# Kernel optimization log

Hardware: AMD Instinct MI355X
Metric: run time of the kernel (lower is better)

## Reference

```python
import jax, jax.numpy as jnp
import numpy as np

X_MIN, X_MAX = -2.0, 2.0


def _pchip_slopes_uniform(y, h):
    # y: [..., K], uniform knot spacing h. Fritsch-Carlson / PCHIP slopes.
    delta = (y[..., 1:] - y[..., :-1]) / h            # [..., K-1]
    dp, dn = delta[..., :-1], delta[..., 1:]          # [..., K-2]
    same_sign = dp * dn > 0
    d_mid = jnp.where(same_sign, 2.0 * dp * dn / (dp + dn + 1e-12), 0.0)

    def _fix_endpoint(d_end, delta0, delta1):
        d_end = jnp.where(d_end * delta0 <= 0, 0.0, d_end)
        d_end = jnp.where((delta0 * delta1 < 0) & (jnp.abs(d_end) > 3.0 * jnp.abs(delta0)),
                          3.0 * delta0, d_end)
        return d_end

    d0 = _fix_endpoint((3.0 * delta[..., 0] - delta[..., 1]) / 2.0, delta[..., 0], delta[..., 1])
    dN = _fix_endpoint((3.0 * delta[..., -1] - delta[..., -2]) / 2.0, delta[..., -1], delta[..., -2])
    return jnp.concatenate([d0[..., None], d_mid, dN[..., None]], axis=-1)


def setup_inputs() -> dict:
    key = jax.random.key(0)
    k1, k2 = jax.random.split(key)
    B, O, D, K = 8192, 64, 64, 64
    x = jax.random.normal(k1, (B, D), dtype=jnp.float32)
    coeffs = 0.01 * jax.random.normal(k2, (O, D, K), dtype=jnp.float32)
    bias = jnp.zeros((O,), dtype=jnp.float32)
    return {"x": x, "coeffs": coeffs, "bias": bias}


def reference(x, coeffs, bias):
    # x: [B, D]; coeffs: [O, D, K]; bias: [O] -> out: [B, O]
    O, D, K = coeffs.shape
    h = (X_MAX - X_MIN) / (K - 1)
    slopes = _pchip_slopes_uniform(coeffs, h)          # [O, D, K]

    t = (x - X_MIN) / h                                # [B, D]
    idx = jnp.clip(jnp.floor(t).astype(jnp.int32), 0, K - 2)
    u = (t - idx)[None]                                # [1, B, D]

    darange = jnp.arange(D)[None, :]                   # broadcasts with idx [B, D]
    y0 = coeffs[:, darange, idx]                       # [O, B, D]
    y1 = coeffs[:, darange, idx + 1]
    d0 = slopes[:, darange, idx]
    d1 = slopes[:, darange, idx + 1]

    u2 = u * u
    u3 = u2 * u
    h00 = 2.0 * u3 - 3.0 * u2 + 1.0
    h10 = u3 - 2.0 * u2 + u
    h01 = -2.0 * u3 + 3.0 * u2
    h11 = u3 - u2
    interp = h00 * y0 + h10 * (h * d0) + h01 * y1 + h11 * (h * d1)  # [O, B, D]

    # linear extrapolation outside [X_MIN, X_MAX]
    left = coeffs[:, :, 0][:, None, :] + slopes[:, :, 0][:, None, :] * (x - X_MIN)[None]
    right = coeffs[:, :, -1][:, None, :] + slopes[:, :, -1][:, None, :] * (x - X_MAX)[None]
    interp = jnp.where((x < X_MIN)[None], left, interp)
    interp = jnp.where((x > X_MAX)[None], right, interp)

    out = interp.sum(axis=-1).T + bias[None, :]        # [B, O]
    return out
```

## Files before the change

kernel.cpp:

```cpp
#include <hip/hip_runtime.h>
#include <hip/hip_fp16.h>
#include <stdint.h>


typedef _Float16 half2v __attribute__((ext_vector_type(2)));

#if defined(__has_builtin)
#if __has_builtin(__builtin_amdgcn_fdot2)
#define HAS_FDOT2 1
#endif
#endif

__device__ __forceinline__ uint32_t h16(float f) {
    return (uint32_t)__half_as_ushort(__float2half(f));
}

__device__ __forceinline__ float dot2acc(uint32_t a_bits, uint32_t b_bits, float acc) {
    half2v a = __builtin_bit_cast(half2v, a_bits);
    half2v b = __builtin_bit_cast(half2v, b_bits);
#ifdef HAS_FDOT2
    return __builtin_amdgcn_fdot2(a, b, acc, false);
#else
    return acc + (float)a.x * (float)b.x + (float)a.y * (float)b.y;
#endif
}

__global__ void build_table(const float* __restrict__ coeffs, uint2* __restrict__ T) {
    const float hf = 4.0f / 63.0f;
    const float inv_hf = 63.0f / 4.0f;
    int d  = blockIdx.x >> 2;
    int ob = (blockIdx.x & 3) << 4;
    __shared__ float Y[16][65];
    int t = threadIdx.x;
    {
        int ol = t >> 4;
        int k4 = (t & 15) << 2;
        const float* src = coeffs + (size_t)(ob + ol) * 4096 + d * 64 + k4;
        float4 v = *(const float4*)src;
        Y[ol][k4 + 0] = v.x; Y[ol][k4 + 1] = v.y;
        Y[ol][k4 + 2] = v.z; Y[ol][k4 + 3] = v.w;
    }
    __syncthreads();
    for (int c = t; c < 1024; c += 256) {
        int ol = c & 15;
        int i  = c >> 4;
        const float* Yr = Y[ol];
        auto delt = [&](int k) -> float { return (Yr[k + 1] - Yr[k]) * inv_hf; };
        auto endslope = [&](float a, float b) -> float {
            float de = (3.0f * a - b) * 0.5f;
            de = (de * a <= 0.0f) ? 0.0f : de;
            de = ((a * b < 0.0f) && (fabsf(de) > 3.0f * fabsf(a))) ? 3.0f * a : de;
            return de;
        };
        auto slope = [&](int k) -> float {
            if (k == 0)  return endslope(delt(0), delt(1));
            if (k == 63) return endslope(delt(62), delt(61));
            float dp = delt(k - 1), dn = delt(k);
            return (dp * dn > 0.0f) ? (2.0f * dp * dn) / (dp + dn + 1e-12f) : 0.0f;
        };
        uint2 pk;
        if (i < 63) {
            float y0 = Yr[i], y1 = Yr[i + 1];
            float di = slope(i), dj = slope(i + 1);
            float c0 = y0;
            float c1 = hf * di;
            float c2 = 3.0f * (y1 - y0) - hf * (2.0f * di + dj);
            float c3 = 2.0f * (y0 - y1) + hf * (di + dj);
            pk.x = (h16(c1) << 16) | h16(c0);
            pk.y = (h16(c3) << 16) | h16(c2);
        } else {
            float yN = Yr[63];
            float dN = slope(63);
            pk.x = (h16(hf * dN) << 16) | h16(yN);
            pk.y = 0u;
        }
        T[(size_t)d * 4096 + i * 64 + (ob + ol)] = pk;
    }
}

__global__ void __launch_bounds__(256) kan_main(const float* __restrict__ x,
                                                const float* __restrict__ bias,
                                                const char* __restrict__ Tb,
                                                float* __restrict__ out) {
    __shared__ uint4 WL[256];
    int t    = threadIdx.x;
    int lane = t & 63;
    int wv   = t >> 6;
    int b    = blockIdx.x * 4 + wv;

    {
        float xv = x[b * 64 + lane];
        float tt = (xv + 2.0f) * 15.75f;
        int i = (int)floorf(tt);
        i = i < 0 ? 0 : (i > 62 ? 62 : i);
        float u = tt - (float)i;
        float w1, w2, w3; uint32_t off;
        if (xv < -2.0f)      { w1 = tt;          w2 = 0.f;    w3 = 0.f;    off = 0u; }
        else if (xv > 2.0f)  { w1 = tt - 63.0f;  w2 = 0.f;    w3 = 0.f;    off = 63u << 9; }
        else                 { w1 = u;           w2 = u * u;  w3 = w2 * u; off = (uint32_t)i << 9; }
        half2v wa; wa.x = (_Float16)1.0f; wa.y = (_Float16)w1;
        half2v wb; wb.x = (_Float16)w2;   wb.y = (_Float16)w3;
        uint32_t full_off = ((uint32_t)lane << 15) | off;
        WL[t] = make_uint4(__builtin_bit_cast(uint32_t, wa),
                           __builtin_bit_cast(uint32_t, wb), full_off, 0u);
    }
    __syncthreads();

    float acc0 = bias[lane];
    float acc1 = 0.0f;
    int laneoff = lane << 3;
    const uint4* wl = &WL[wv << 6];
    #pragma unroll 8
    for (int d = 0; d < 64; ++d) {
        uint4 q = wl[d];
        uint32_t off = __builtin_amdgcn_readfirstlane(q.z);
        uint2 c = *(const uint2*)(Tb + off + laneoff);
        acc0 = dot2acc(q.x, c.x, acc0);
        acc1 = dot2acc(q.y, c.y, acc1);
    }
    out[b * 64 + lane] = acc0 + acc1;
}

extern "C" void kernel_launch(void* const* d_in, const int* in_sizes, int n_in,
                              void* d_out, int out_size, void* d_ws, size_t ws_size,
                              hipStream_t stream) {
    const float* x      = (const float*)d_in[0];
    const float* coeffs = (const float*)d_in[1];
    const float* bias   = (const float*)d_in[2];
    float* out = (float*)d_out;

    uint2* T = (uint2*)d_ws;
    build_table<<<dim3(256), dim3(256), 0, stream>>>(coeffs, T);
    kan_main<<<dim3(2048), dim3(256), 0, stream>>>(x, bias, (const char*)d_ws, out);
}
```

Measured before the change: 79.06 us.

## Split each batch row's D reduction across four waves using readlane broadcasts

Each block now handles one batch row instead of four. Its four waves each cover 16 of the 64 input dimensions and combine partial sums through shared memory. Per-dimension weights and offsets are broadcast with readlane instead of being staged in LDS, which removes the LDS weight table and the pre-loop barrier. This raises the grid to 8192 blocks, shortens each wave's serial dependency chain and fully unrolls it, at the cost of a final barrier, an LDS reduction and three idle waves during the store.

```diff
diff --git a/kernel.cpp b/kernel.cpp
--- a/kernel.cpp
+++ b/kernel.cpp
@@ -82,12 +82,13 @@
                                                 const float* __restrict__ bias,
                                                 const char* __restrict__ Tb,
                                                 float* __restrict__ out) {
-    __shared__ uint4 WL[256];
+    __shared__ float R[4][64];
     int t    = threadIdx.x;
     int lane = t & 63;
     int wv   = t >> 6;
-    int b    = blockIdx.x * 4 + wv;
+    int b    = blockIdx.x;
 
+    uint32_t wa_bits, wb_bits, off_full;
     {
         float xv = x[b * 64 + lane];
         float tt = (xv + 2.0f) * 15.75f;
@@ -100,25 +101,32 @@
         else                 { w1 = u;           w2 = u * u;  w3 = w2 * u; off = (uint32_t)i << 9; }
         half2v wa; wa.x = (_Float16)1.0f; wa.y = (_Float16)w1;
         half2v wb; wb.x = (_Float16)w2;   wb.y = (_Float16)w3;
-        uint32_t full_off = ((uint32_t)lane << 15) | off;
-        WL[t] = make_uint4(__builtin_bit_cast(uint32_t, wa),
-                           __builtin_bit_cast(uint32_t, wb), full_off, 0u);
+        wa_bits  = __builtin_bit_cast(uint32_t, wa);
+        wb_bits  = __builtin_bit_cast(uint32_t, wb);
+        off_full = ((uint32_t)lane << 15) | off;
     }
-    __syncthreads();
 
-    float acc0 = bias[lane];
+    float acc0 = 0.0f;
     float acc1 = 0.0f;
     int laneoff = lane << 3;
-    const uint4* wl = &WL[wv << 6];
-    #pragma unroll 8
-    for (int d = 0; d < 64; ++d) {
-        uint4 q = wl[d];
-        uint32_t off = __builtin_amdgcn_readfirstlane(q.z);
+    int lb = __builtin_amdgcn_readfirstlane(wv << 4);
+    #pragma unroll
+    for (int j = 0; j < 16; ++j) {
+        int src = lb + j;
+        uint32_t qa  = (uint32_t)__builtin_amdgcn_readlane((int)wa_bits,  src);
+        uint32_t qb  = (uint32_t)__builtin_amdgcn_readlane((int)wb_bits,  src);
+        uint32_t off = (uint32_t)__builtin_amdgcn_readlane((int)off_full, src);
         uint2 c = *(const uint2*)(Tb + off + laneoff);
-        acc0 = dot2acc(q.x, c.x, acc0);
-        acc1 = dot2acc(q.y, c.y, acc1);
+        acc0 = dot2acc(qa, c.x, acc0);
+        acc1 = dot2acc(qb, c.y, acc1);
     }
-    out[b * 64 + lane] = acc0 + acc1;
+
+    R[wv][lane] = acc0 + acc1;
+    __syncthreads();
+    if (wv == 0) {
+        float r = R[0][lane] + R[1][lane] + R[2][lane] + R[3][lane] + bias[lane];
+        out[b * 64 + lane] = r;
+    }
 }
 
 extern "C" void kernel_launch(void* const* d_in, const int* in_sizes, int n_in,
@@ -131,5 +139,5 @@
 
     uint2* T = (uint2*)d_ws;
     build_table<<<dim3(256), dim3(256), 0, stream>>>(coeffs, T);
-    kan_main<<<dim3(2048), dim3(256), 0, stream>>>(x, bias, (const char*)d_ws, out);
+    kan_main<<<dim3(8192), dim3(256), 0, stream>>>(x, bias, (const char*)d_ws, out);
 }
```

Measured after the change: 80.24 us. About the same (+1.5%).

## Stage coefficient table slices in LDS and split D across blocks with reduction

Applied to the files above, without the earlier changes.

The main kernel now splits the D dimension into 8 groups per block. Each block copies 2-dimension slices of the packed Hermite table into LDS with global_load_lds, then evaluates 256 batch rows against that LDS-resident table instead of gathering from global memory per element. Partial sums per D group go to a workspace and a new reduce kernel adds them together with the bias. The intent is to replace scattered global/L2 gathers with LDS reads and more reuse per block. The cost is an extra kernel launch, extra traffic for the partials, 64KB+ of LDS per block (lower occupancy), and barriers around each table reload.

```diff
diff --git a/kernel.cpp b/kernel.cpp
--- a/kernel.cpp
+++ b/kernel.cpp
@@ -78,47 +78,104 @@
     }
 }
 
-__global__ void __launch_bounds__(256) kan_main(const float* __restrict__ x,
-                                                const float* __restrict__ bias,
+__global__ void __launch_bounds__(512) kan_main(const float* __restrict__ x,
                                                 const char* __restrict__ Tb,
-                                                float* __restrict__ out) {
-    __shared__ uint4 WL[256];
-    int t    = threadIdx.x;
-    int lane = t & 63;
-    int wv   = t >> 6;
-    int b    = blockIdx.x * 4 + wv;
+                                                float* __restrict__ part) {
+    __shared__ char  TL[65536];
+    __shared__ uint4 REC[256][8];
+
+    const int t     = threadIdx.x;
+    const int lane  = t & 63;
+    const int wv    = t >> 6;
+    const int p     = blockIdx.x & 7;
+    const int btile = blockIdx.x >> 3;
+    const int dg    = p << 3;
+    const int bbase = btile << 8;
 
     {
-        float xv = x[b * 64 + lane];
+        const char* src = Tb + ((size_t)dg << 15);
+        #pragma unroll
+        for (int r = 0; r < 8; ++r) {
+            __builtin_amdgcn_global_load_lds(
+                (const uint32_t*)(src + t * 16 + r * 8192),
+                (uint32_t*)(TL + t * 16 + r * 8192), 16, 0, 0);
+        }
+    }
+
+    #pragma unroll
+    for (int k = 0; k < 4; ++k) {
+        int r  = t + (k << 9);
+        int bl = r >> 3;
+        int dl = r & 7;
+        float xv = x[(bbase + bl) * 64 + dg + dl];
         float tt = (xv + 2.0f) * 15.75f;
         int i = (int)floorf(tt);
         i = i < 0 ? 0 : (i > 62 ? 62 : i);
         float u = tt - (float)i;
         float w1, w2, w3; uint32_t off;
-        if (xv < -2.0f)      { w1 = tt;          w2 = 0.f;    w3 = 0.f;    off = 0u; }
-        else if (xv > 2.0f)  { w1 = tt - 63.0f;  w2 = 0.f;    w3 = 0.f;    off = 63u << 9; }
-        else                 { w1 = u;           w2 = u * u;  w3 = w2 * u; off = (uint32_t)i << 9; }
+        if (xv < -2.0f)      { w1 = tt;          w2 = 0.f;    w3 = 0.f;     off = 0u; }
+        else if (xv > 2.0f)  { w1 = tt - 63.0f;  w2 = 0.f;    w3 = 0.f;     off = 63u << 9; }
+        else                 { w1 = u;           w2 = u * u;  w3 = w2 * u;  off = (uint32_t)i << 9; }
         half2v wa; wa.x = (_Float16)1.0f; wa.y = (_Float16)w1;
         half2v wb; wb.x = (_Float16)w2;   wb.y = (_Float16)w3;
-        uint32_t full_off = ((uint32_t)lane << 15) | off;
-        WL[t] = make_uint4(__builtin_bit_cast(uint32_t, wa),
-                           __builtin_bit_cast(uint32_t, wb), full_off, 0u);
+        REC[bl][dl] = make_uint4(__builtin_bit_cast(uint32_t, wa),
+                                 __builtin_bit_cast(uint32_t, wb), off, 0u);
     }
     __syncthreads();
 
-    float acc0 = bias[lane];
-    float acc1 = 0.0f;
-    int laneoff = lane << 3;
-    const uint4* wl = &WL[wv << 6];
-    #pragma unroll 8
-    for (int d = 0; d < 64; ++d) {
-        uint4 q = wl[d];
-        uint32_t off = __builtin_amdgcn_readfirstlane(q.z);
-        uint2 c = *(const uint2*)(Tb + off + laneoff);
-        acc0 = dot2acc(q.x, c.x, acc0);
-        acc1 = dot2acc(q.y, c.y, acc1);
+    float acc[32];
+    #pragma unroll
+    for (int j = 0; j < 32; ++j) acc[j] = 0.0f;
+
+    const int laneoff = lane << 3;
+    for (int c = 0; c < 4; ++c) {
+        const int c2 = c << 1;
+        #pragma unroll
+        for (int j = 0; j < 32; ++j) {
+            int bl = (wv << 5) + j;
+            uint4 r0 = REC[bl][c2 + 0];
+            uint4 r1 = REC[bl][c2 + 1];
+            uint2 q0 = *(const uint2*)(TL + (r0.z + laneoff));
+            uint2 q1 = *(const uint2*)(TL + (32768 + r1.z + laneoff));
+            acc[j] = dot2acc(r0.x, q0.x, acc[j]);
+            acc[j] = dot2acc(r0.y, q0.y, acc[j]);
+            acc[j] = dot2acc(r1.x, q1.x, acc[j]);
+            acc[j] = dot2acc(r1.y, q1.y, acc[j]);
+        }
+        if (c < 3) {
+            __syncthreads();
+            const char* src = Tb + ((size_t)(dg + c2 + 2) << 15);
+            #pragma unroll
+            for (int r = 0; r < 8; ++r) {
+                __builtin_amdgcn_global_load_lds(
+                    (const uint32_t*)(src + t * 16 + r * 8192),
+                    (uint32_t*)(TL + t * 16 + r * 8192), 16, 0, 0);
+            }
+            __syncthreads();
+        }
     }
-    out[b * 64 + lane] = acc0 + acc1;
+
+    float* dst = part + ((size_t)p * 8192 + bbase + (wv << 5)) * 64 + lane;
+    #pragma unroll
+    for (int j = 0; j < 32; ++j) {
+        dst[j * 64] = acc[j];
+    }
+}
+
+__global__ void __launch_bounds__(256) kan_reduce(const float* __restrict__ part,
+                                                  const float* __restrict__ bias,
+                                                  float* __restrict__ out) {
+    int idx = blockIdx.x * 256 + threadIdx.x;
+    const float4* p4 = (const float4*)part;
+    float4 s = p4[idx];
+    #pragma unroll
+    for (int pp = 1; pp < 8; ++pp) {
+        float4 v = p4[(size_t)pp * 131072 + idx];
+        s.x += v.x; s.y += v.y; s.z += v.z; s.w += v.w;
+    }
+    float4 bv = ((const float4*)bias)[idx & 15];
+    s.x += bv.x; s.y += bv.y; s.z += bv.z; s.w += bv.w;
+    ((float4*)out)[idx] = s;
 }
 
 extern "C" void kernel_launch(void* const* d_in, const int* in_sizes, int n_in,
@@ -129,7 +186,10 @@
     const float* bias   = (const float*)d_in[2];
     float* out = (float*)d_out;
 
-    uint2* T = (uint2*)d_ws;
+    uint2* T    = (uint2*)d_ws;
+    float* part = (float*)((char*)d_ws + (2u << 20));
+
     build_table<<<dim3(256), dim3(256), 0, stream>>>(coeffs, T);
-    kan_main<<<dim3(2048), dim3(256), 0, stream>>>(x, bias, (const char*)d_ws, out);
+    kan_main<<<dim3(256), dim3(512), 0, stream>>>(x, (const char*)T, part);
+    kan_reduce<<<dim3(512), dim3(256), 0, stream>>>(part, bias, out);
 }
```

Result: slower. 93.62 us (+18.4%).

## Compute two outputs per lane with 16-byte table loads and drop block barrier

Applied to the files above, without the earlier changes.

Each wave now processes two batch rows, one per half-wave. Each lane computes two adjacent outputs from a single 16-byte table load, and the grid is halved. Each wave reads only the LDS weight rows it wrote itself, so the block-wide __syncthreads is removed. This aims to cut the number of load instructions and the barrier cost. In exchange, each load address is uniform only per half-wave rather than per wave, and correctness now relies on in-wave ordering of LDS writes and reads.

```diff
diff --git a/kernel.cpp b/kernel.cpp
--- a/kernel.cpp
+++ b/kernel.cpp
@@ -82,43 +82,52 @@
                                                 const float* __restrict__ bias,
                                                 const char* __restrict__ Tb,
                                                 float* __restrict__ out) {
-    __shared__ uint4 WL[256];
-    int t    = threadIdx.x;
-    int lane = t & 63;
-    int wv   = t >> 6;
-    int b    = blockIdx.x * 4 + wv;
+    __shared__ uint4 WL[8][64];
+    const int t     = threadIdx.x;
+    const int lane  = t & 63;
+    const int wv    = t >> 6;
+    const int half  = lane >> 5;
+    const int ol    = lane & 31;
+    const int bbase = blockIdx.x << 3;
 
-    {
-        float xv = x[b * 64 + lane];
+    #pragma unroll
+    for (int k = 0; k < 2; ++k) {
+        int bl = (wv << 1) + k;
+        float xv = x[(bbase + bl) * 64 + lane];
         float tt = (xv + 2.0f) * 15.75f;
         int i = (int)floorf(tt);
         i = i < 0 ? 0 : (i > 62 ? 62 : i);
         float u = tt - (float)i;
         float w1, w2, w3; uint32_t off;
-        if (xv < -2.0f)      { w1 = tt;          w2 = 0.f;    w3 = 0.f;    off = 0u; }
-        else if (xv > 2.0f)  { w1 = tt - 63.0f;  w2 = 0.f;    w3 = 0.f;    off = 63u << 9; }
-        else                 { w1 = u;           w2 = u * u;  w3 = w2 * u; off = (uint32_t)i << 9; }
+        if (xv < -2.0f)      { w1 = tt;          w2 = 0.f;    w3 = 0.f;     off = 0u; }
+        else if (xv > 2.0f)  { w1 = tt - 63.0f;  w2 = 0.f;    w3 = 0.f;     off = 63u << 9; }
+        else                 { w1 = u;           w2 = u * u;  w3 = w2 * u;  off = (uint32_t)i << 9; }
         half2v wa; wa.x = (_Float16)1.0f; wa.y = (_Float16)w1;
         half2v wb; wb.x = (_Float16)w2;   wb.y = (_Float16)w3;
-        uint32_t full_off = ((uint32_t)lane << 15) | off;
-        WL[t] = make_uint4(__builtin_bit_cast(uint32_t, wa),
-                           __builtin_bit_cast(uint32_t, wb), full_off, 0u);
+        WL[bl][lane] = make_uint4(__builtin_bit_cast(uint32_t, wa),
+                                  __builtin_bit_cast(uint32_t, wb),
+                                  ((uint32_t)lane << 15) | off, 0u);
     }
-    __syncthreads();
 
-    float acc0 = bias[lane];
-    float acc1 = 0.0f;
-    int laneoff = lane << 3;
-    const uint4* wl = &WL[wv << 6];
+    const uint4* rbase = &WL[(wv << 1) + half][0];
+    const int laneoff = ol << 4;
+    float ae0 = 0.0f, ae1 = 0.0f, ao0 = 0.0f, ao1 = 0.0f;
     #pragma unroll 8
     for (int d = 0; d < 64; ++d) {
-        uint4 q = wl[d];
-        uint32_t off = __builtin_amdgcn_readfirstlane(q.z);
-        uint2 c = *(const uint2*)(Tb + off + laneoff);
-        acc0 = dot2acc(q.x, c.x, acc0);
-        acc1 = dot2acc(q.y, c.y, acc1);
+        uint4 r = rbase[d];
+        uint4 q = *(const uint4*)(Tb + r.z + laneoff);
+        ae0 = dot2acc(r.x, q.x, ae0);
+        ae1 = dot2acc(r.y, q.y, ae1);
+        ao0 = dot2acc(r.x, q.z, ao0);
+        ao1 = dot2acc(r.y, q.w, ao1);
     }
-    out[b * 64 + lane] = acc0 + acc1;
+
+    float2 bv = ((const float2*)bias)[ol];
+    float2 res;
+    res.x = ae0 + ae1 + bv.x;
+    res.y = ao0 + ao1 + bv.y;
+    int b = bbase + (wv << 1) + half;
+    ((float2*)(out + (size_t)b * 64))[ol] = res;
 }
 
 extern "C" void kernel_launch(void* const* d_in, const int* in_sizes, int n_in,
@@ -131,5 +140,5 @@
 
     uint2* T = (uint2*)d_ws;
     build_table<<<dim3(256), dim3(256), 0, stream>>>(coeffs, T);
-    kan_main<<<dim3(2048), dim3(256), 0, stream>>>(x, bias, (const char*)d_ws, out);
+    kan_main<<<dim3(1024), dim3(256), 0, stream>>>(x, bias, (const char*)d_ws, out);
 }
```

After: 74.02 us (median of 2 runs). -6.4%, faster.
